# Performance work log

Hardware: AMD Instinct MI355X
Metric: run time of the kernel (lower is better)

## Reference

```python
import jax, jax.numpy as jnp
import numpy as np

B, S, E, H = 4, 8192, 1024, 16
D = E // H  # head_dim = 64


def setup_inputs() -> dict:
    key = jax.random.key(0)
    ks = jax.random.split(key, 9)
    s = 0.02
    return {
        "x": jax.random.normal(ks[0], (B, S, E), dtype=jnp.float32),
        "Wq": jax.random.normal(ks[1], (D, E), dtype=jnp.float32) * s,
        "bq": jax.random.normal(ks[2], (D,), dtype=jnp.float32) * s,
        "Wk": jax.random.normal(ks[3], (D, E), dtype=jnp.float32) * s,
        "bk": jax.random.normal(ks[4], (D,), dtype=jnp.float32) * s,
        "Wv": jax.random.normal(ks[5], (D, E), dtype=jnp.float32) * s,
        "bv": jax.random.normal(ks[6], (D,), dtype=jnp.float32) * s,
        "Wo": jax.random.normal(ks[7], (E, E), dtype=jnp.float32) * s,
        "bo": jax.random.normal(ks[8], (E,), dtype=jnp.float32) * s,
    }


def reference(x, Wq, bq, Wk, bk, Wv, bv, Wo, bo):
    b, s, e = x.shape
    d = Wq.shape[0]          # head_dim (projections map embed_dim -> head_dim)
    h = e // d               # num_heads
    # torch Linear: y = x @ W.T + b ; projected shape [B, S, d]
    # view(B, -1, h, d) on [B, S, d] => effective seq S' = S // h (faithful to source)
    def split_heads(t):
        return t.reshape(b, -1, h, d).transpose(0, 2, 1, 3)  # [B, H, S', D]
    q = split_heads(x @ Wq.T + bq)
    k = split_heads(x @ Wk.T + bk)
    v = split_heads(x @ Wv.T + bv)
    scores = jnp.einsum('bhqd,bhkd->bhqk', q, k) / np.sqrt(d).astype(jnp.float32)
    attn = jax.nn.softmax(scores, axis=-1)  # dropout=0.0 => identity
    ctx = jnp.einsum('bhqk,bhkd->bhqd', attn, v)
    ctx = ctx.transpose(0, 2, 1, 3).reshape(b, -1, e)  # [B, S', E]
    return ctx @ Wo.T + bo
```

## Files before the change

kernel.cpp:

```cpp
#include <hip/hip_runtime.h>
#include <hip/hip_bf16.h>


typedef unsigned short u16;
typedef __attribute__((ext_vector_type(8))) short short8;
typedef __attribute__((ext_vector_type(4))) float f32x4;

#define VMWAIT(N) asm volatile("s_waitcnt vmcnt(" #N ")" ::: "memory")
#define MEMFENCE() asm volatile("" ::: "memory")
#define BAR() __builtin_amdgcn_s_barrier()

__device__ inline u16 f2bf(float f) {
    union { float f; unsigned u; } v; v.f = f;
    unsigned u = v.u;
    return (u16)((u + 0x7fffu + ((u >> 16) & 1u)) >> 16);
}
__device__ inline unsigned pack_bf2(float a, float b) {
    union { __hip_bfloat162 h; unsigned u; } v;
    v.h = __float22bfloat162_rn(float2{a, b});
    return v.u;
}
__device__ __forceinline__ void gld16(void* lds, const void* gptr) {
    __builtin_amdgcn_global_load_lds(
        (const __attribute__((address_space(1))) unsigned int*)gptr,
        (__attribute__((address_space(3))) unsigned int*)lds,
        16, 0, 0);
}

__global__ __launch_bounds__(256) void convw(
    const float* __restrict__ Wq, const float* __restrict__ bq,
    const float* __restrict__ Wk, const float* __restrict__ bk,
    const float* __restrict__ Wv, const float* __restrict__ bv,
    const float* __restrict__ Wo,
    u16* __restrict__ Wqkv, float* __restrict__ qkvb, u16* __restrict__ Wob)
{
    const int idx = blockIdx.x * 256 + threadIdx.x;
    Wob[idx] = f2bf(Wo[idx]);
    if (idx < 196608) {
        const int row = idx >> 10, k = idx & 1023;
        float v = (row < 64)  ? Wq[row * 1024 + k] * 0.125f
                : (row < 128) ? Wk[(row - 64) * 1024 + k]
                              : Wv[(row - 128) * 1024 + k];
        Wqkv[idx] = f2bf(v);
    }
    if (idx < 192) {
        qkvb[idx] = (idx < 64) ? bq[idx] * 0.125f
                  : (idx < 128) ? bk[idx - 64] : bv[idx - 128];
    }
}

__global__ __launch_bounds__(256, 2) void qkv_gemm(
    const float* __restrict__ X, const u16* __restrict__ W,
    const float* __restrict__ bias, u16* __restrict__ Out)
{
    __shared__ short8 Bs[3][1536];

    const int tid = threadIdx.x;
    const int lane = tid & 63, wid = tid >> 6;
    const int q = lane >> 4, r = lane & 15;
    const int wm = wid >> 1, wn = wid & 1;
    const long m0 = (long)blockIdx.x * 64;

    const u16* wp[6];
    #pragma unroll
    for (int i = 0; i < 6; ++i) {
        const int p = wid * 6 + i, kk2 = p / 12, nt = p % 12;
        wp[i] = W + (long)(nt * 16 + r) * 1024 + kk2 * 32 + q * 8;
    }

    const float* px0 = X + (m0 + wm * 32 + r) * 1024 + q * 8;
    const float* px1 = px0 + 16 * 1024;

    f32x4 acc[2][6] = {};
    float4 a[3][2][4];

#define LOADA(s, j) do {                                            \
        a[s][0][0] = *(const float4*)(px0 + (j) * 64);              \
        a[s][0][1] = *(const float4*)(px0 + (j) * 64 + 4);          \
        a[s][0][2] = *(const float4*)(px0 + (j) * 64 + 32);         \
        a[s][0][3] = *(const float4*)(px0 + (j) * 64 + 36);         \
        a[s][1][0] = *(const float4*)(px1 + (j) * 64);              \
        a[s][1][1] = *(const float4*)(px1 + (j) * 64 + 4);          \
        a[s][1][2] = *(const float4*)(px1 + (j) * 64 + 32);         \
        a[s][1][3] = *(const float4*)(px1 + (j) * 64 + 36);         \
    } while (0)

#define STAGE(j) do {                                               \
        _Pragma("unroll")                                           \
        for (int i = 0; i < 6; ++i)                                 \
            gld16(&Bs[(j) % 3][(wid * 6 + i) * 64], wp[i] + (j) * 64); \
    } while (0)

    LOADA(0, 0);  MEMFENCE();
    STAGE(0);     MEMFENCE();
    LOADA(1, 1);  MEMFENCE();
    STAGE(1);     MEMFENCE();
    LOADA(2, 2);  MEMFENCE();

    #pragma unroll
    for (int k = 0; k < 16; ++k) {
        const int slot = k % 3;
        if (k + 2 < 16) { STAGE(k + 2); MEMFENCE(); }
        if (k < 14)      VMWAIT(28);
        else if (k == 14) VMWAIT(14);
        else             VMWAIT(0);
        BAR();
        MEMFENCE();
        #pragma unroll
        for (int kk2 = 0; kk2 < 2; ++kk2) {
            union { short8 s; unsigned u[4]; } af0, af1;
            af0.u[0] = pack_bf2(a[slot][0][kk2 * 2].x, a[slot][0][kk2 * 2].y);
            af0.u[1] = pack_bf2(a[slot][0][kk2 * 2].z, a[slot][0][kk2 * 2].w);
            af0.u[2] = pack_bf2(a[slot][0][kk2 * 2 + 1].x, a[slot][0][kk2 * 2 + 1].y);
            af0.u[3] = pack_bf2(a[slot][0][kk2 * 2 + 1].z, a[slot][0][kk2 * 2 + 1].w);
            af1.u[0] = pack_bf2(a[slot][1][kk2 * 2].x, a[slot][1][kk2 * 2].y);
            af1.u[1] = pack_bf2(a[slot][1][kk2 * 2].z, a[slot][1][kk2 * 2].w);
            af1.u[2] = pack_bf2(a[slot][1][kk2 * 2 + 1].x, a[slot][1][kk2 * 2 + 1].y);
            af1.u[3] = pack_bf2(a[slot][1][kk2 * 2 + 1].z, a[slot][1][kk2 * 2 + 1].w);
            #pragma unroll
            for (int j = 0; j < 6; ++j) {
                const short8 bf = Bs[slot][(kk2 * 12 + wn * 6 + j) * 64 + lane];
                acc[0][j] = __builtin_amdgcn_mfma_f32_16x16x32_bf16(
                    af0.s, bf, acc[0][j], 0, 0, 0);
                acc[1][j] = __builtin_amdgcn_mfma_f32_16x16x32_bf16(
                    af1.s, bf, acc[1][j], 0, 0, 0);
            }
        }
        MEMFENCE();
        if (k + 3 < 16) { LOADA(slot, k + 3); MEMFENCE(); }
        BAR();
    }
#undef LOADA
#undef STAGE

    u16* lds0 = (u16*)&Bs[0][0];
    #pragma unroll
    for (int j = 0; j < 6; ++j) {
        const int col = wn * 96 + j * 16 + r;
        const float badd = bias[col];
        #pragma unroll
        for (int mf = 0; mf < 2; ++mf)
            #pragma unroll
            for (int e = 0; e < 4; ++e)
                lds0[(wm * 32 + mf * 16 + q * 4 + e) * 192 + col] =
                    f2bf(acc[mf][j][e] + badd);
    }
    asm volatile("s_waitcnt lgkmcnt(0)" ::: "memory");
    BAR();
    const short8* l8 = (const short8*)lds0;
    u16* ob = Out + m0 * 192;
    #pragma unroll
    for (int s = 0; s < 6; ++s) {
        short8 v = l8[tid + s * 256];
        *(short8*)(ob + (long)(tid + s * 256) * 8) = v;
    }
}

__global__ __launch_bounds__(256) void vtrans(
    const u16* __restrict__ qkv, u16* __restrict__ Vt)
{
    __shared__ u16 T[64][68];
    const int bh = blockIdx.x, b = bh >> 4, h = bh & 15;
    const int i0 = blockIdx.y * 64;
    const int tid = threadIdx.x;

    #pragma unroll
    for (int it = 0; it < 2; ++it) {
        const int c = tid + 256 * it;
        const int il = c >> 3, d8 = (c & 7) * 8;
        short8 v = *(const short8*)(qkv +
            ((long)b * 8192 + (long)(i0 + il) * 16 + h) * 192 + 128 + d8);
        #pragma unroll
        for (int j = 0; j < 8; ++j) T[d8 + j][il] = (u16)v[j];
    }
    __syncthreads();
    #pragma unroll
    for (int it = 0; it < 2; ++it) {
        const int c = tid + 256 * it;
        const int dl = c >> 3, i8 = (c & 7) * 8;
        short8 o;
        #pragma unroll
        for (int j = 0; j < 8; ++j) o[j] = (short)T[dl][i8 + j];
        *(short8*)(Vt + ((long)bh * 64 + dl) * 512 + i0 + i8) = o;
    }
}

__global__ __launch_bounds__(256) void attn_flash(
    const u16* __restrict__ qkv, const u16* __restrict__ Vt,
    u16* __restrict__ ctx)
{
    __shared__ short8 Ks[2][512];
    __shared__ short8 Vs[2][512];
    __shared__ u16 Plds[4][16 * 72];

    const int tid = threadIdx.x, lane = tid & 63, wid = tid >> 6;
    const int q = lane >> 4, r = lane & 15;
    const int qt = blockIdx.x;
    const int bh = blockIdx.y;
    const int b = bh >> 4, h = bh & 15;
    const long qrowbase = (long)b * 8192 + h;

    short8 Qf0, Qf1;
    {
        const int i = qt * 64 + wid * 16 + r;
        const u16* p = qkv + (qrowbase + (long)i * 16) * 192 + q * 8;
        Qf0 = *(const short8*)(p);
        Qf1 = *(const short8*)(p + 32);
    }

    const u16* kbase = qkv + (qrowbase + (long)(wid * 16 + r) * 16) * 192
                           + 64 + q * 8;
    const u16* vbase = Vt + ((long)bh * 64 + wid * 16 + r) * 512 + q * 8;

    gld16(&Ks[0][wid * 64],       kbase);
    gld16(&Ks[0][256 + wid * 64], kbase + 32);
    gld16(&Vs[0][wid * 64],       vbase);
    gld16(&Vs[0][256 + wid * 64], vbase + 32);

    f32x4 O[4] = {};
    float mrun = -1e30f, lrun = 0.f;
    u16* Pw = &Plds[wid][0];

    for (int c = 0; c < 8; ++c) {
        const int j0 = c * 64, buf = c & 1;
        if (c < 7) {
            const u16* kp = kbase + (long)(j0 + 64) * 3072;
            const u16* vp = vbase + j0 + 64;
            gld16(&Ks[buf ^ 1][wid * 64],       kp);
            gld16(&Ks[buf ^ 1][256 + wid * 64], kp + 32);
            gld16(&Vs[buf ^ 1][wid * 64],       vp);
            gld16(&Vs[buf ^ 1][256 + wid * 64], vp + 32);
            VMWAIT(4);
        } else {
            VMWAIT(0);
        }
        BAR();
        MEMFENCE();
        f32x4 S[4];
        #pragma unroll
        for (int ct = 0; ct < 4; ++ct) {
            f32x4 s = {};
            s = __builtin_amdgcn_mfma_f32_16x16x32_bf16(
                Ks[buf][ct * 64 + lane], Qf0, s, 0, 0, 0);
            s = __builtin_amdgcn_mfma_f32_16x16x32_bf16(
                Ks[buf][256 + ct * 64 + lane], Qf1, s, 0, 0, 0);
            S[ct] = s;
        }
        float mc = -1e30f;
        #pragma unroll
        for (int ct = 0; ct < 4; ++ct)
            mc = fmaxf(mc, fmaxf(fmaxf(S[ct][0], S[ct][1]),
                                 fmaxf(S[ct][2], S[ct][3])));
        mc = fmaxf(mc, __shfl_xor(mc, 16, 64));
        mc = fmaxf(mc, __shfl_xor(mc, 32, 64));
        const float mnew = fmaxf(mrun, mc);
        const float alpha = __expf(mrun - mnew);
        mrun = mnew;
        float se = 0.f;
        #pragma unroll
        for (int ct = 0; ct < 4; ++ct)
            #pragma unroll
            for (int e = 0; e < 4; ++e) {
                const float pv = __expf(S[ct][e] - mnew);
                S[ct][e] = pv; se += pv;
            }
        se += __shfl_xor(se, 16, 64);
        se += __shfl_xor(se, 32, 64);
        lrun = lrun * alpha + se;
        #pragma unroll
        for (int nt = 0; nt < 4; ++nt)
            #pragma unroll
            for (int e = 0; e < 4; ++e) O[nt][e] *= alpha;
        #pragma unroll
        for (int ct = 0; ct < 4; ++ct) {
            uint2 d;
            d.x = pack_bf2(S[ct][0], S[ct][1]);
            d.y = pack_bf2(S[ct][2], S[ct][3]);
            *(uint2*)(Pw + r * 72 + ct * 16 + q * 4) = d;
        }
        short8 Pf0 = *(const short8*)(Pw + r * 72 + q * 8);
        short8 Pf1 = *(const short8*)(Pw + r * 72 + 32 + q * 8);
        #pragma unroll
        for (int nt = 0; nt < 4; ++nt) {
            O[nt] = __builtin_amdgcn_mfma_f32_16x16x32_bf16(
                Vs[buf][nt * 64 + lane], Pf0, O[nt], 0, 0, 0);
            O[nt] = __builtin_amdgcn_mfma_f32_16x16x32_bf16(
                Vs[buf][256 + nt * 64 + lane], Pf1, O[nt], 0, 0, 0);
        }
        MEMFENCE();
        BAR();
    }

    const float inv = 1.0f / lrun;
    const long i = qt * 64 + wid * 16 + r;
    u16* po = ctx + ((long)b * 512 + i) * 1024 + h * 64;
    #pragma unroll
    for (int nt = 0; nt < 4; ++nt) {
        uint2 d;
        d.x = pack_bf2(O[nt][0] * inv, O[nt][1] * inv);
        d.y = pack_bf2(O[nt][2] * inv, O[nt][3] * inv);
        *(uint2*)(po + nt * 16 + q * 4) = d;
    }
}

__global__ __launch_bounds__(256) void gemm_o(
    const u16* __restrict__ A, const u16* __restrict__ B,
    const float* __restrict__ bias, float* __restrict__ C)
{
    __shared__ short8 As[2][512];
    __shared__ short8 Bs[2][512];

    const int tid = threadIdx.x;
    const int lane = tid & 63, wid = tid >> 6;
    const int q = lane >> 4, r = lane & 15;
    const long m0 = (long)blockIdx.x * 64, n0 = (long)blockIdx.y * 64;
    const int wm = wid >> 1, wn = wid & 1;

    const u16* ap[2];
    const u16* bp[2];
    #pragma unroll
    for (int i = 0; i < 2; ++i) {
        const int t = wid * 2 + i, f = t >> 2, mt = t & 3;
        ap[i] = A + (m0 + mt * 16 + r) * 1024 + f * 32 + q * 8;
        bp[i] = B + (n0 + mt * 16 + r) * 1024 + f * 32 + q * 8;
    }

    #pragma unroll
    for (int i = 0; i < 2; ++i) {
        gld16(&As[0][(wid * 2 + i) * 64], ap[i]);
        gld16(&Bs[0][(wid * 2 + i) * 64], bp[i]);
    }

    f32x4 acc[2][2] = {};

    for (int k0 = 0; k0 < 1024; k0 += 64) {
        const int buf = (k0 >> 6) & 1;
        if (k0 + 64 < 1024) {
            #pragma unroll
            for (int i = 0; i < 2; ++i) {
                gld16(&As[buf ^ 1][(wid * 2 + i) * 64], ap[i] + k0 + 64);
                gld16(&Bs[buf ^ 1][(wid * 2 + i) * 64], bp[i] + k0 + 64);
            }
            VMWAIT(4);
        } else {
            VMWAIT(0);
        }
        BAR();
        MEMFENCE();
        #pragma unroll
        for (int f = 0; f < 2; ++f) {
            short8 af0 = As[buf][f * 256 + (wm * 2 + 0) * 64 + lane];
            short8 af1 = As[buf][f * 256 + (wm * 2 + 1) * 64 + lane];
            short8 bf0 = Bs[buf][f * 256 + (wn * 2 + 0) * 64 + lane];
            short8 bf1 = Bs[buf][f * 256 + (wn * 2 + 1) * 64 + lane];
            acc[0][0] = __builtin_amdgcn_mfma_f32_16x16x32_bf16(af0, bf0, acc[0][0], 0, 0, 0);
            acc[0][1] = __builtin_amdgcn_mfma_f32_16x16x32_bf16(af0, bf1, acc[0][1], 0, 0, 0);
            acc[1][0] = __builtin_amdgcn_mfma_f32_16x16x32_bf16(af1, bf0, acc[1][0], 0, 0, 0);
            acc[1][1] = __builtin_amdgcn_mfma_f32_16x16x32_bf16(af1, bf1, acc[1][1], 0, 0, 0);
        }
        MEMFENCE();
        BAR();
    }

    #pragma unroll
    for (int i = 0; i < 2; ++i)
        #pragma unroll
        for (int j = 0; j < 2; ++j) {
            const long col = n0 + (wn * 2 + j) * 16 + r;
            const float badd = bias[col];
            #pragma unroll
            for (int e = 0; e < 4; ++e) {
                const long row = m0 + (wm * 2 + i) * 16 + q * 4 + e;
                C[row * 1024 + col] = acc[i][j][e] + badd;
            }
        }
}

extern "C" void kernel_launch(void* const* d_in, const int* in_sizes, int n_in,
                              void* d_out, int out_size, void* d_ws, size_t ws_size,
                              hipStream_t stream)
{
    const float* x  = (const float*)d_in[0];
    const float* Wq = (const float*)d_in[1];
    const float* bq = (const float*)d_in[2];
    const float* Wk = (const float*)d_in[3];
    const float* bk = (const float*)d_in[4];
    const float* Wv = (const float*)d_in[5];
    const float* bv = (const float*)d_in[6];
    const float* Wo = (const float*)d_in[7];
    const float* bo = (const float*)d_in[8];
    float* out = (float*)d_out;
    char* ws = (char*)d_ws;

    u16*   qkv  = (u16*)(ws);
    u16*   Vt   = (u16*)(ws + 12582912);
    u16*   Wqkv = (u16*)(ws + 16777216);
    u16*   Wob  = (u16*)(ws + 17170432);
    float* qkvb = (float*)(ws + 19267584);
    u16*   ctx  = (u16*)(ws + 19268352);

    convw<<<4096, 256, 0, stream>>>(Wq, bq, Wk, bk, Wv, bv, Wo, Wqkv, qkvb, Wob);
    qkv_gemm<<<512, 256, 0, stream>>>(x, Wqkv, qkvb, qkv);
    vtrans<<<dim3(64, 8), 256, 0, stream>>>(qkv, Vt);
    attn_flash<<<dim3(8, 64), 256, 0, stream>>>(qkv, Vt, ctx);
    gemm_o<<<dim3(32, 16), 256, 0, stream>>>(ctx, Wob, bo, out);
}
```

Baseline: 263.5 us.

## Split QKV GEMM block across 8 waves with one 16-row fragment each

The QKV projection kernel goes from 256 to 512 threads per block. Each wave now owns a 16-row M fragment instead of 32 rows, which halves per-thread accumulators, A-operand registers and B-tile staging loads. The goal is more waves in flight to hide the fp32 X global-load latency and bf16 conversion. The trade-off is more barrier participants and a lower MFMA-to-load ratio per wave, while the same 64-row block tile and LDS footprint are kept.

```diff
diff --git a/kernel.cpp b/kernel.cpp
--- a/kernel.cpp
+++ b/kernel.cpp
@@ -49,7 +49,7 @@
     }
 }
 
-__global__ __launch_bounds__(256, 2) void qkv_gemm(
+__global__ __launch_bounds__(512, 4) void qkv_gemm(
     const float* __restrict__ X, const u16* __restrict__ W,
     const float* __restrict__ bias, u16* __restrict__ Out)
 {
@@ -61,34 +61,29 @@
     const int wm = wid >> 1, wn = wid & 1;
     const long m0 = (long)blockIdx.x * 64;
 
-    const u16* wp[6];
-    #pragma unroll
-    for (int i = 0; i < 6; ++i) {
-        const int p = wid * 6 + i, kk2 = p / 12, nt = p % 12;
+    const u16* wp[3];
+    #pragma unroll
+    for (int i = 0; i < 3; ++i) {
+        const int p = wid * 3 + i, kk2 = p / 12, nt = p % 12;
         wp[i] = W + (long)(nt * 16 + r) * 1024 + kk2 * 32 + q * 8;
     }
 
-    const float* px0 = X + (m0 + wm * 32 + r) * 1024 + q * 8;
-    const float* px1 = px0 + 16 * 1024;
-
-    f32x4 acc[2][6] = {};
-    float4 a[3][2][4];
+    const float* px = X + (m0 + wm * 16 + r) * 1024 + q * 8;
+
+    f32x4 acc[6] = {};
+    float4 a[3][4];
 
 #define LOADA(s, j) do {                                            \
-        a[s][0][0] = *(const float4*)(px0 + (j) * 64);              \
-        a[s][0][1] = *(const float4*)(px0 + (j) * 64 + 4);          \
-        a[s][0][2] = *(const float4*)(px0 + (j) * 64 + 32);         \
-        a[s][0][3] = *(const float4*)(px0 + (j) * 64 + 36);         \
-        a[s][1][0] = *(const float4*)(px1 + (j) * 64);              \
-        a[s][1][1] = *(const float4*)(px1 + (j) * 64 + 4);          \
-        a[s][1][2] = *(const float4*)(px1 + (j) * 64 + 32);         \
-        a[s][1][3] = *(const float4*)(px1 + (j) * 64 + 36);         \
+        a[s][0] = *(const float4*)(px + (j) * 64);                  \
+        a[s][1] = *(const float4*)(px + (j) * 64 + 4);              \
+        a[s][2] = *(const float4*)(px + (j) * 64 + 32);             \
+        a[s][3] = *(const float4*)(px + (j) * 64 + 36);             \
     } while (0)
 
 #define STAGE(j) do {                                               \
         _Pragma("unroll")                                           \
-        for (int i = 0; i < 6; ++i)                                 \
-            gld16(&Bs[(j) % 3][(wid * 6 + i) * 64], wp[i] + (j) * 64); \
+        for (int i = 0; i < 3; ++i)                                 \
+            gld16(&Bs[(j) % 3][(wid * 3 + i) * 64], wp[i] + (j) * 64); \
     } while (0)
 
     LOADA(0, 0);  MEMFENCE();
@@ -101,29 +96,23 @@
     for (int k = 0; k < 16; ++k) {
         const int slot = k % 3;
         if (k + 2 < 16) { STAGE(k + 2); MEMFENCE(); }
-        if (k < 14)      VMWAIT(28);
-        else if (k == 14) VMWAIT(14);
-        else             VMWAIT(0);
+        if (k < 14)       VMWAIT(14);
+        else if (k == 14) VMWAIT(7);
+        else              VMWAIT(0);
         BAR();
         MEMFENCE();
         #pragma unroll
         for (int kk2 = 0; kk2 < 2; ++kk2) {
-            union { short8 s; unsigned u[4]; } af0, af1;
-            af0.u[0] = pack_bf2(a[slot][0][kk2 * 2].x, a[slot][0][kk2 * 2].y);
-            af0.u[1] = pack_bf2(a[slot][0][kk2 * 2].z, a[slot][0][kk2 * 2].w);
-            af0.u[2] = pack_bf2(a[slot][0][kk2 * 2 + 1].x, a[slot][0][kk2 * 2 + 1].y);
-            af0.u[3] = pack_bf2(a[slot][0][kk2 * 2 + 1].z, a[slot][0][kk2 * 2 + 1].w);
-            af1.u[0] = pack_bf2(a[slot][1][kk2 * 2].x, a[slot][1][kk2 * 2].y);
-            af1.u[1] = pack_bf2(a[slot][1][kk2 * 2].z, a[slot][1][kk2 * 2].w);
-            af1.u[2] = pack_bf2(a[slot][1][kk2 * 2 + 1].x, a[slot][1][kk2 * 2 + 1].y);
-            af1.u[3] = pack_bf2(a[slot][1][kk2 * 2 + 1].z, a[slot][1][kk2 * 2 + 1].w);
+            union { short8 s; unsigned u[4]; } af;
+            af.u[0] = pack_bf2(a[slot][kk2 * 2].x, a[slot][kk2 * 2].y);
+            af.u[1] = pack_bf2(a[slot][kk2 * 2].z, a[slot][kk2 * 2].w);
+            af.u[2] = pack_bf2(a[slot][kk2 * 2 + 1].x, a[slot][kk2 * 2 + 1].y);
+            af.u[3] = pack_bf2(a[slot][kk2 * 2 + 1].z, a[slot][kk2 * 2 + 1].w);
             #pragma unroll
             for (int j = 0; j < 6; ++j) {
                 const short8 bf = Bs[slot][(kk2 * 12 + wn * 6 + j) * 64 + lane];
-                acc[0][j] = __builtin_amdgcn_mfma_f32_16x16x32_bf16(
-                    af0.s, bf, acc[0][j], 0, 0, 0);
-                acc[1][j] = __builtin_amdgcn_mfma_f32_16x16x32_bf16(
-                    af1.s, bf, acc[1][j], 0, 0, 0);
+                acc[j] = __builtin_amdgcn_mfma_f32_16x16x32_bf16(
+                    af.s, bf, acc[j], 0, 0, 0);
             }
         }
         MEMFENCE();
@@ -139,20 +128,17 @@
         const int col = wn * 96 + j * 16 + r;
         const float badd = bias[col];
         #pragma unroll
-        for (int mf = 0; mf < 2; ++mf)
-            #pragma unroll
-            for (int e = 0; e < 4; ++e)
-                lds0[(wm * 32 + mf * 16 + q * 4 + e) * 192 + col] =
-                    f2bf(acc[mf][j][e] + badd);
+        for (int e = 0; e < 4; ++e)
+            lds0[(wm * 16 + q * 4 + e) * 192 + col] = f2bf(acc[j][e] + badd);
     }
     asm volatile("s_waitcnt lgkmcnt(0)" ::: "memory");
     BAR();
     const short8* l8 = (const short8*)lds0;
     u16* ob = Out + m0 * 192;
     #pragma unroll
-    for (int s = 0; s < 6; ++s) {
-        short8 v = l8[tid + s * 256];
-        *(short8*)(ob + (long)(tid + s * 256) * 8) = v;
+    for (int s = 0; s < 3; ++s) {
+        short8 v = l8[tid + s * 512];
+        *(short8*)(ob + (long)(tid + s * 512) * 8) = v;
     }
 }
 
@@ -400,7 +386,7 @@
     u16*   ctx  = (u16*)(ws + 19268352);
 
     convw<<<4096, 256, 0, stream>>>(Wq, bq, Wk, bk, Wv, bv, Wo, Wqkv, qkvb, Wob);
-    qkv_gemm<<<512, 256, 0, stream>>>(x, Wqkv, qkvb, qkv);
+    qkv_gemm<<<512, 512, 0, stream>>>(x, Wqkv, qkvb, qkv);
     vtrans<<<dim3(64, 8), 256, 0, stream>>>(qkv, Vt);
     attn_flash<<<dim3(8, 64), 256, 0, stream>>>(qkv, Vt, ctx);
     gemm_o<<<dim3(32, 16), 256, 0, stream>>>(ctx, Wob, bo, out);
```

Result: no change. 263.1 us (-0.2%).
